# Performance work log

Measured on AMD Instinct MI355X. Metric: run time of the kernel, lower is better.

## Reference

```python
import jax, jax.numpy as jnp
import numpy as np

B, T, D, F, E, K = 2, 1024, 1024, 2048, 8, 2

def setup_inputs() -> dict:
    key = jax.random.key(0)
    ks = jax.random.split(key, 9)
    s = 0.02
    return {
        "states": jax.random.normal(ks[0], (B, T, D), dtype=jnp.float32),
        "Wg": jax.random.normal(ks[1], (D, E), dtype=jnp.float32) * s,
        "W_in": jax.random.normal(ks[2], (E, D, F), dtype=jnp.float32) * s,
        "b_in": jnp.zeros((E, F), dtype=jnp.float32),
        "W_scale": jax.random.normal(ks[3], (E, D, F), dtype=jnp.float32) * s,
        "b_scale": jnp.zeros((E, F), dtype=jnp.float32),
        "W_out": jax.random.normal(ks[4], (E, F, D), dtype=jnp.float32) * s,
        "b_out": jnp.zeros((E, D), dtype=jnp.float32),
        "num_selected": K,
    }

def reference(states, Wg, W_in, b_in, W_scale, b_scale, W_out, b_out, num_selected):
    b, t, d = states.shape
    x = states.reshape(-1, d)                      # [N, D]
    n = x.shape[0]
    # router: softmax over experts, then top-k + renormalize
    probs = jax.nn.softmax(x @ Wg, axis=-1)        # [N, E]
    topw, topi = jax.lax.top_k(probs, num_selected)  # [N, K]
    topw = topw / topw.sum(axis=-1, keepdims=True)
    # dense combine weights [N, E]: zero except selected experts
    w_full = jnp.zeros_like(probs).at[jnp.arange(n)[:, None], topi].set(topw)
    # gated-GELU expert MLPs, batched over experts
    h = jnp.einsum('nd,edf->enf', x, W_in) + b_in[:, None, :]       # [E, N, F]
    s = jnp.einsum('nd,edf->enf', x, W_scale) + b_scale[:, None, :]
    inner = jax.nn.gelu(h, approximate=False) * s                    # exact GELU (torch default)
    y = jnp.einsum('enf,efd->end', inner, W_out) + b_out[:, None, :]  # [E, N, D]
    out = jnp.einsum('end,ne->nd', y, w_full)                         # weighted combine
    return out.reshape(b, t, d)
```

## Files before the change

kernel.cpp:

```cpp
#include <hip/hip_runtime.h>
#include <hip/hip_bf16.h>
#include <math.h>

#define N_TOK 2048
#define DIM   1024
#define FF    2048
#define NEXP  8
#define NSLOT (N_TOK * 2)

typedef __attribute__((ext_vector_type(8))) short short8;
typedef __attribute__((ext_vector_type(4))) float f32x4;
typedef _Float16 half_t;
typedef __attribute__((ext_vector_type(4))) _Float16 h16x4;

__device__ __forceinline__ unsigned short f2bf(float f) {
    unsigned int u = __float_as_uint(f);
    u += 0x7FFFu + ((u >> 16) & 1u);
    return (unsigned short)(u >> 16);
}

#define GLOAD_LDS16(g, l) \
    __builtin_amdgcn_global_load_lds((const __attribute__((address_space(1))) unsigned int*)(g), \
                                     (__attribute__((address_space(3))) unsigned int*)(l), 16, 0, 0)

__global__ __launch_bounds__(256) void k_router(const float* __restrict__ x,
        const float* __restrict__ Wg, int* __restrict__ hdr,
        int* __restrict__ tok_e, float* __restrict__ tok_w) {
    int wave = threadIdx.x >> 6, lane = threadIdx.x & 63;
    int t = blockIdx.x * 4 + wave;
    float acc[NEXP];
#pragma unroll
    for (int e = 0; e < NEXP; ++e) acc[e] = 0.f;
    const float* xr = x + (size_t)t * DIM;
    for (int d = lane; d < DIM; d += 64) {
        float xv = xr[d];
        const float* wr = Wg + d * NEXP;
#pragma unroll
        for (int e = 0; e < NEXP; ++e) acc[e] += xv * wr[e];
    }
#pragma unroll
    for (int off = 32; off > 0; off >>= 1) {
#pragma unroll
        for (int e = 0; e < NEXP; ++e) acc[e] += __shfl_down(acc[e], off);
    }
    if (lane == 0) {
        int e0 = 0;
#pragma unroll
        for (int e = 1; e < NEXP; ++e) if (acc[e] > acc[e0]) e0 = e;
        int e1 = -1;
#pragma unroll
        for (int e = 0; e < NEXP; ++e) {
            if (e == e0) continue;
            if (e1 < 0 || acc[e] > acc[e1]) e1 = e;
        }
        float w0 = 1.f / (1.f + expf(acc[e1] - acc[e0]));
        tok_e[2 * t] = e0; tok_e[2 * t + 1] = e1;
        tok_w[2 * t] = w0; tok_w[2 * t + 1] = 1.f - w0;
        atomicAdd(&hdr[e0], 1);
        atomicAdd(&hdr[e1], 1);
    }
}

__global__ void k_scan(int* hdr) {
    if (threadIdx.x == 0 && blockIdx.x == 0) {
        int s = 0;
        for (int e = 0; e < NEXP; ++e) {
            hdr[16 + e] = s;
            hdr[8 + e]  = s;
            s += hdr[e];
        }
        hdr[24] = s;
    }
}

__global__ __launch_bounds__(256) void k_assign(const float* __restrict__ x,
        int* __restrict__ hdr, const int* __restrict__ tok_e,
        int* __restrict__ tok_slot, unsigned short* __restrict__ xg) {
    __shared__ int sh[2];
    int t = blockIdx.x;
    if (threadIdx.x == 0) {
        int e0 = tok_e[2 * t], e1 = tok_e[2 * t + 1];
        int p0 = atomicAdd(&hdr[8 + e0], 1);
        int p1 = atomicAdd(&hdr[8 + e1], 1);
        tok_slot[2 * t] = p0; tok_slot[2 * t + 1] = p1;
        sh[0] = p0; sh[1] = p1;
    }
    __syncthreads();
    int s0 = sh[0], s1 = sh[1];
    const float4* xr = (const float4*)(x + (size_t)t * DIM);
    float4 v = xr[threadIdx.x];
    ushort4 b;
    b.x = f2bf(v.x); b.y = f2bf(v.y); b.z = f2bf(v.z); b.w = f2bf(v.w);
    ((ushort4*)(xg + (size_t)s0 * DIM))[threadIdx.x] = b;
    ((ushort4*)(xg + (size_t)s1 * DIM))[threadIdx.x] = b;
}

__global__ __launch_bounds__(256, 4) void k_expert_hs(
        const unsigned short* __restrict__ xg,
        const float* __restrict__ Win, const float* __restrict__ Wsc,
        const float* __restrict__ b_in, const float* __restrict__ b_sc,
        const int* __restrict__ hdr, unsigned short* __restrict__ inner) {
    int e = blockIdx.z;
    int cnt = hdr[e];
    int mtile = blockIdx.y;
    if (mtile * 128 >= cnt) return;
    int base = hdr[16 + e];
    int f0 = blockIdx.x * 64;

    __shared__ unsigned short As[128 * 32];
    __shared__ unsigned short Bh[4 * 64 * 8];
    __shared__ unsigned short Bs[4 * 64 * 8];

    int tid = threadIdx.x;
    int wave = tid >> 6, lane = tid & 63;
    int lr = lane & 15, lq = lane >> 4;
    int wm = (wave >> 1) * 64, wf = (wave & 1) * 32;

    f32x4 acch[4][2], accs[4][2];
#pragma unroll
    for (int mi = 0; mi < 4; ++mi)
#pragma unroll
        for (int fi = 0; fi < 2; ++fi) {
            acch[mi][fi] = (f32x4){0.f, 0.f, 0.f, 0.f};
            accs[mi][fi] = (f32x4){0.f, 0.f, 0.f, 0.f};
        }

    const unsigned short* Arow = xg + (size_t)(base + mtile * 128) * DIM;
    int arow = wave * 16 + (lane >> 2);
    int akk  = (lane & 3) * 8;

    int bf = tid & 63, bkq = tid >> 6;
    const float* ph_base = Win + (size_t)e * DIM * FF + f0 + bf;
    const float* ps_base = Wsc + (size_t)e * DIM * FF + f0 + bf;

    unsigned hv[4], sv[4];
    {
        const float* ph = ph_base + (size_t)(bkq * 8) * FF;
        const float* ps = ps_base + (size_t)(bkq * 8) * FF;
#pragma unroll
        for (int j = 0; j < 4; ++j) {
            hv[j] = (unsigned)f2bf(ph[(size_t)(2 * j) * FF]) |
                    ((unsigned)f2bf(ph[(size_t)(2 * j + 1) * FF]) << 16);
            sv[j] = (unsigned)f2bf(ps[(size_t)(2 * j) * FF]) |
                    ((unsigned)f2bf(ps[(size_t)(2 * j + 1) * FF]) << 16);
        }
    }

    for (int k0 = 0; k0 < DIM; k0 += 32) {
        __syncthreads();
        const unsigned short* gA = Arow + (size_t)arow * DIM + k0 + akk;
        GLOAD_LDS16(gA, &As[(wave * 16) * 32]);
        GLOAD_LDS16(gA + (size_t)64 * DIM, &As[(64 + wave * 16) * 32]);
        *(uint4*)&Bh[(bkq * 64 + bf) * 8] = make_uint4(hv[0], hv[1], hv[2], hv[3]);
        *(uint4*)&Bs[(bkq * 64 + bf) * 8] = make_uint4(sv[0], sv[1], sv[2], sv[3]);
        __syncthreads();

        unsigned hvN[4], svN[4];
        bool more = (k0 + 32 < DIM);
        if (more) {
            const float* ph = ph_base + (size_t)(k0 + 32 + bkq * 8) * FF;
            const float* ps = ps_base + (size_t)(k0 + 32 + bkq * 8) * FF;
#pragma unroll
            for (int j = 0; j < 4; ++j) {
                hvN[j] = (unsigned)f2bf(ph[(size_t)(2 * j) * FF]) |
                         ((unsigned)f2bf(ph[(size_t)(2 * j + 1) * FF]) << 16);
                svN[j] = (unsigned)f2bf(ps[(size_t)(2 * j) * FF]) |
                         ((unsigned)f2bf(ps[(size_t)(2 * j + 1) * FF]) << 16);
            }
        }

        short8 af[4], bhf[2], bsf[2];
#pragma unroll
        for (int mi = 0; mi < 4; ++mi)
            af[mi] = *(const short8*)&As[(wm + mi * 16 + lr) * 32 + lq * 8];
#pragma unroll
        for (int fi = 0; fi < 2; ++fi) {
            bhf[fi] = *(const short8*)&Bh[(lq * 64 + wf + fi * 16 + lr) * 8];
            bsf[fi] = *(const short8*)&Bs[(lq * 64 + wf + fi * 16 + lr) * 8];
        }
#pragma unroll
        for (int mi = 0; mi < 4; ++mi)
#pragma unroll
            for (int fi = 0; fi < 2; ++fi) {
                acch[mi][fi] = __builtin_amdgcn_mfma_f32_16x16x32_bf16(
                    af[mi], bhf[fi], acch[mi][fi], 0, 0, 0);
                accs[mi][fi] = __builtin_amdgcn_mfma_f32_16x16x32_bf16(
                    af[mi], bsf[fi], accs[mi][fi], 0, 0, 0);
            }
        if (more) {
#pragma unroll
            for (int j = 0; j < 4; ++j) { hv[j] = hvN[j]; sv[j] = svN[j]; }
        }
    }

#pragma unroll
    for (int fi = 0; fi < 2; ++fi) {
        int f = f0 + wf + fi * 16 + lr;
        float bi = b_in[e * FF + f];
        float bs2 = b_sc[e * FF + f];
#pragma unroll
        for (int mi = 0; mi < 4; ++mi) {
#pragma unroll
            for (int r = 0; r < 4; ++r) {
                int rl = wm + mi * 16 + lq * 4 + r;
                int grow = mtile * 128 + rl;
                if (grow < cnt) {
                    float h = acch[mi][fi][r] + bi;
                    float s = accs[mi][fi][r] + bs2;
                    float g = 0.5f * h * (1.f + erff(h * 0.70710678f));
                    inner[(size_t)(base + grow) * FF + f] = f2bf(g * s);
                }
            }
        }
    }
}

__global__ __launch_bounds__(256, 4) void k_expert_out(
        const unsigned short* __restrict__ inner,
        const float* __restrict__ Wout,
        const int* __restrict__ hdr, half_t* __restrict__ pbuf) {
    int e = blockIdx.z & 7;
    int ks = blockIdx.z >> 3;
    int cnt = hdr[e];
    int mtile = blockIdx.y;
    if (mtile * 128 >= cnt) return;
    int base = hdr[16 + e];
    int d0 = blockIdx.x * 128;

    __shared__ unsigned short As[128 * 32];
    __shared__ unsigned short Bt[4 * 128 * 8];

    int tid = threadIdx.x;
    int wave = tid >> 6, lane = tid & 63;
    int lr = lane & 15, lq = lane >> 4;
    int wm = (wave >> 1) * 64, wn = (wave & 1) * 64;

    f32x4 acc[4][4];
#pragma unroll
    for (int mi = 0; mi < 4; ++mi)
#pragma unroll
        for (int ni = 0; ni < 4; ++ni) acc[mi][ni] = (f32x4){0.f, 0.f, 0.f, 0.f};

    const unsigned short* Arow = inner + (size_t)(base + mtile * 128) * FF;
    int arow = wave * 16 + (lane >> 2);
    int akk  = (lane & 3) * 8;

    int bd = tid & 127, bq = tid >> 7;
    const float* Wb = Wout + (size_t)e * FF * DIM + d0 + bd;

    int kbeg = ks * (FF / 2), kend = kbeg + FF / 2;

    unsigned wv[8];
    {
        const float* pw = Wb + (size_t)(kbeg + bq * 16) * DIM;
#pragma unroll
        for (int j = 0; j < 8; ++j)
            wv[j] = (unsigned)f2bf(pw[(size_t)(2 * j) * DIM]) |
                    ((unsigned)f2bf(pw[(size_t)(2 * j + 1) * DIM]) << 16);
    }

    for (int k0 = kbeg; k0 < kend; k0 += 32) {
        __syncthreads();
        const unsigned short* gA = Arow + (size_t)arow * FF + k0 + akk;
        GLOAD_LDS16(gA, &As[(wave * 16) * 32]);
        GLOAD_LDS16(gA + (size_t)64 * FF, &As[(64 + wave * 16) * 32]);
        *(uint4*)&Bt[((2 * bq) * 128 + bd) * 8]     = make_uint4(wv[0], wv[1], wv[2], wv[3]);
        *(uint4*)&Bt[((2 * bq + 1) * 128 + bd) * 8] = make_uint4(wv[4], wv[5], wv[6], wv[7]);
        __syncthreads();

        unsigned wvN[8];
        bool more = (k0 + 32 < kend);
        if (more) {
            const float* pw = Wb + (size_t)(k0 + 32 + bq * 16) * DIM;
#pragma unroll
            for (int j = 0; j < 8; ++j)
                wvN[j] = (unsigned)f2bf(pw[(size_t)(2 * j) * DIM]) |
                         ((unsigned)f2bf(pw[(size_t)(2 * j + 1) * DIM]) << 16);
        }

        short8 af[4], bfm[4];
#pragma unroll
        for (int mi = 0; mi < 4; ++mi)
            af[mi] = *(const short8*)&As[(wm + mi * 16 + lr) * 32 + lq * 8];
#pragma unroll
        for (int ni = 0; ni < 4; ++ni)
            bfm[ni] = *(const short8*)&Bt[(lq * 128 + wn + ni * 16 + lr) * 8];
#pragma unroll
        for (int mi = 0; mi < 4; ++mi)
#pragma unroll
            for (int ni = 0; ni < 4; ++ni)
                acc[mi][ni] = __builtin_amdgcn_mfma_f32_16x16x32_bf16(
                    af[mi], bfm[ni], acc[mi][ni], 0, 0, 0);
        if (more) {
#pragma unroll
            for (int j = 0; j < 8; ++j) wv[j] = wvN[j];
        }
    }

    half_t* P = pbuf + (size_t)ks * NSLOT * DIM;
#pragma unroll
    for (int ni = 0; ni < 4; ++ni) {
        int d = d0 + wn + ni * 16 + lr;
#pragma unroll
        for (int mi = 0; mi < 4; ++mi) {
#pragma unroll
            for (int r = 0; r < 4; ++r) {
                int rl = wm + mi * 16 + lq * 4 + r;
                int grow = mtile * 128 + rl;
                if (grow < cnt)
                    P[(size_t)(base + grow) * DIM + d] = (half_t)acc[mi][ni][r];
            }
        }
    }
}

__global__ __launch_bounds__(256) void k_combine(const half_t* __restrict__ pbuf,
        const int* __restrict__ tok_slot, const int* __restrict__ tok_e,
        const float* __restrict__ tok_w, const float* __restrict__ b_out,
        float* __restrict__ out) {
    int t = blockIdx.x;
    int d = threadIdx.x * 4;
    int s0 = tok_slot[2 * t], s1 = tok_slot[2 * t + 1];
    int e0 = tok_e[2 * t], e1 = tok_e[2 * t + 1];
    float w0 = tok_w[2 * t], w1 = tok_w[2 * t + 1];
    const half_t* pA = pbuf;
    const half_t* pB = pbuf + (size_t)NSLOT * DIM;
    h16x4 a0 = *(const h16x4*)&pA[(size_t)s0 * DIM + d];
    h16x4 a1 = *(const h16x4*)&pB[(size_t)s0 * DIM + d];
    h16x4 c0 = *(const h16x4*)&pA[(size_t)s1 * DIM + d];
    h16x4 c1 = *(const h16x4*)&pB[(size_t)s1 * DIM + d];
    float4 b0 = *(const float4*)&b_out[e0 * DIM + d];
    float4 b1 = *(const float4*)&b_out[e1 * DIM + d];
    float4 r;
    r.x = w0 * ((float)a0.x + (float)a1.x + b0.x) + w1 * ((float)c0.x + (float)c1.x + b1.x);
    r.y = w0 * ((float)a0.y + (float)a1.y + b0.y) + w1 * ((float)c0.y + (float)c1.y + b1.y);
    r.z = w0 * ((float)a0.z + (float)a1.z + b0.z) + w1 * ((float)c0.z + (float)c1.z + b1.z);
    r.w = w0 * ((float)a0.w + (float)a1.w + b0.w) + w1 * ((float)c0.w + (float)c1.w + b1.w);
    *(float4*)&out[(size_t)t * DIM + d] = r;
}

extern "C" void kernel_launch(void* const* d_in, const int* in_sizes, int n_in,
                              void* d_out, int out_size, void* d_ws, size_t ws_size,
                              hipStream_t stream) {
    (void)in_sizes; (void)n_in; (void)out_size; (void)ws_size;
    const float* x    = (const float*)d_in[0];
    const float* Wg   = (const float*)d_in[1];
    const float* Win  = (const float*)d_in[2];
    const float* b_in = (const float*)d_in[3];
    const float* Wsc  = (const float*)d_in[4];
    const float* b_sc = (const float*)d_in[5];
    const float* Wout = (const float*)d_in[6];
    const float* b_out= (const float*)d_in[7];
    float* out = (float*)d_out;

    char* ws = (char*)d_ws;
    int*   hdr      = (int*)ws;
    int*   tok_e    = (int*)(ws + 256);
    float* tok_w    = (float*)(ws + 16640);
    int*   tok_slot = (int*)(ws + 33024);
    unsigned short* xg    = (unsigned short*)(ws + 65792);
    unsigned short* inner = (unsigned short*)(ws + 65792 + 8388608);
    half_t* pbuf = (half_t*)(ws + 65792 + 8388608 + 16777216);

    hipMemsetAsync(hdr, 0, 256, stream);
    k_router<<<dim3(N_TOK / 4), dim3(256), 0, stream>>>(x, Wg, hdr, tok_e, tok_w);
    k_scan<<<dim3(1), dim3(64), 0, stream>>>(hdr);
    k_assign<<<dim3(N_TOK), dim3(256), 0, stream>>>(x, hdr, tok_e, tok_slot, xg);
    k_expert_hs<<<dim3(FF / 64, 16, NEXP), dim3(256), 0, stream>>>(xg, Win, Wsc, b_in, b_sc, hdr, inner);
    k_expert_out<<<dim3(DIM / 128, 16, NEXP * 2), dim3(256), 0, stream>>>(inner, Wout, hdr, pbuf);
    k_combine<<<dim3(N_TOK), dim3(256), 0, stream>>>(pbuf, tok_slot, tok_e, tok_w, b_out, out);
}
```

Before: 472.0 us.

## Pre-transpose expert weights to bf16 and stream all GEMM operands via direct LDS loads

Adds a transpose kernel that converts W_in, W_scale and W_out from fp32 to K-major bf16 copies in workspace. Both expert GEMMs then load A and B tiles with global_load_lds into a fragment-ordered shared layout, replacing strided per-element fp32 loads with register conversion. This is meant to cut scattered, uncoalesced weight reads and conversion work inside the GEMM loops. The cost is an extra pass that reads all weights and writes bf16 copies on every call, plus a larger workspace.

```diff
diff --git a/kernel.cpp b/kernel.cpp
--- a/kernel.cpp
+++ b/kernel.cpp
@@ -95,9 +95,41 @@
     ((ushort4*)(xg + (size_t)s1 * DIM))[threadIdx.x] = b;
 }
 
+__global__ __launch_bounds__(256) void k_transpose(
+        const float* __restrict__ Win, const float* __restrict__ Wsc,
+        const float* __restrict__ Wout, unsigned short* __restrict__ WinT,
+        unsigned short* __restrict__ WscT, unsigned short* __restrict__ WoutT) {
+    int z = blockIdx.z, tsel = z >> 3, e = z & 7;
+    int R = (tsel == 2) ? FF : DIM;
+    int C = (tsel == 2) ? DIM : FF;
+    int tr0 = blockIdx.y * 64, tc0 = blockIdx.x * 64;
+    if (tr0 >= R || tc0 >= C) return;
+    const float* src = ((tsel == 0) ? Win : (tsel == 1) ? Wsc : Wout) + (size_t)e * DIM * FF;
+    unsigned short* dst = ((tsel == 0) ? WinT : (tsel == 1) ? WscT : WoutT) + (size_t)e * DIM * FF;
+    __shared__ unsigned short T[64][68];
+    int t = threadIdx.x, tr = t >> 4, tc = (t & 15) * 4;
+#pragma unroll
+    for (int i = 0; i < 4; ++i) {
+        int r = tr + i * 16;
+        float4 v = *(const float4*)&src[(size_t)(tr0 + r) * C + tc0 + tc];
+        ushort4 b;
+        b.x = f2bf(v.x); b.y = f2bf(v.y); b.z = f2bf(v.z); b.w = f2bf(v.w);
+        *(ushort4*)&T[r][tc] = b;
+    }
+    __syncthreads();
+    int r4 = (t & 15) * 4;
+#pragma unroll
+    for (int i = 0; i < 4; ++i) {
+        int c = tr + i * 16;
+        ushort4 b;
+        b.x = T[r4][c]; b.y = T[r4 + 1][c]; b.z = T[r4 + 2][c]; b.w = T[r4 + 3][c];
+        *(ushort4*)&dst[(size_t)(tc0 + c) * R + tr0 + r4] = b;
+    }
+}
+
 __global__ __launch_bounds__(256, 4) void k_expert_hs(
         const unsigned short* __restrict__ xg,
-        const float* __restrict__ Win, const float* __restrict__ Wsc,
+        const unsigned short* __restrict__ WinT, const unsigned short* __restrict__ WscT,
         const float* __restrict__ b_in, const float* __restrict__ b_sc,
         const int* __restrict__ hdr, unsigned short* __restrict__ inner) {
     int e = blockIdx.z;
@@ -107,9 +139,9 @@
     int base = hdr[16 + e];
     int f0 = blockIdx.x * 64;
 
-    __shared__ unsigned short As[128 * 32];
-    __shared__ unsigned short Bh[4 * 64 * 8];
-    __shared__ unsigned short Bs[4 * 64 * 8];
+    __shared__ unsigned short As[8 * 512];
+    __shared__ unsigned short Bh[4 * 512];
+    __shared__ unsigned short Bs[4 * 512];
 
     int tid = threadIdx.x;
     int wave = tid >> 6, lane = tid & 63;
@@ -126,57 +158,36 @@
         }
 
     const unsigned short* Arow = xg + (size_t)(base + mtile * 128) * DIM;
-    int arow = wave * 16 + (lane >> 2);
-    int akk  = (lane & 3) * 8;
-
-    int bf = tid & 63, bkq = tid >> 6;
-    const float* ph_base = Win + (size_t)e * DIM * FF + f0 + bf;
-    const float* ps_base = Wsc + (size_t)e * DIM * FF + f0 + bf;
-
-    unsigned hv[4], sv[4];
-    {
-        const float* ph = ph_base + (size_t)(bkq * 8) * FF;
-        const float* ps = ps_base + (size_t)(bkq * 8) * FF;
-#pragma unroll
-        for (int j = 0; j < 4; ++j) {
-            hv[j] = (unsigned)f2bf(ph[(size_t)(2 * j) * FF]) |
-                    ((unsigned)f2bf(ph[(size_t)(2 * j + 1) * FF]) << 16);
-            sv[j] = (unsigned)f2bf(ps[(size_t)(2 * j) * FF]) |
-                    ((unsigned)f2bf(ps[(size_t)(2 * j + 1) * FF]) << 16);
-        }
-    }
+    const unsigned short* gA0 = Arow + (size_t)(wave * 16 + lr) * DIM + lq * 8;
+    const unsigned short* gA1 = gA0 + (size_t)64 * DIM;
+    const unsigned short* gBh = WinT + (size_t)e * DIM * FF + (size_t)(f0 + wave * 16 + lr) * DIM + lq * 8;
+    const unsigned short* gBs = WscT + (size_t)e * DIM * FF + (size_t)(f0 + wave * 16 + lr) * DIM + lq * 8;
+    unsigned short* lA0 = As + wave * 512;
+    unsigned short* lA1 = As + (4 + wave) * 512;
+    unsigned short* lBh = Bh + wave * 512;
+    unsigned short* lBs = Bs + wave * 512;
+
+    const unsigned short* rA  = As + (wm >> 4) * 512 + lq * 128 + lr * 8;
+    const unsigned short* rBh = Bh + (wf >> 4) * 512 + lq * 128 + lr * 8;
+    const unsigned short* rBs = Bs + (wf >> 4) * 512 + lq * 128 + lr * 8;
 
     for (int k0 = 0; k0 < DIM; k0 += 32) {
         __syncthreads();
-        const unsigned short* gA = Arow + (size_t)arow * DIM + k0 + akk;
-        GLOAD_LDS16(gA, &As[(wave * 16) * 32]);
-        GLOAD_LDS16(gA + (size_t)64 * DIM, &As[(64 + wave * 16) * 32]);
-        *(uint4*)&Bh[(bkq * 64 + bf) * 8] = make_uint4(hv[0], hv[1], hv[2], hv[3]);
-        *(uint4*)&Bs[(bkq * 64 + bf) * 8] = make_uint4(sv[0], sv[1], sv[2], sv[3]);
+        GLOAD_LDS16(gA0, lA0);
+        GLOAD_LDS16(gA1, lA1);
+        GLOAD_LDS16(gBh, lBh);
+        GLOAD_LDS16(gBs, lBs);
         __syncthreads();
-
-        unsigned hvN[4], svN[4];
-        bool more = (k0 + 32 < DIM);
-        if (more) {
-            const float* ph = ph_base + (size_t)(k0 + 32 + bkq * 8) * FF;
-            const float* ps = ps_base + (size_t)(k0 + 32 + bkq * 8) * FF;
-#pragma unroll
-            for (int j = 0; j < 4; ++j) {
-                hvN[j] = (unsigned)f2bf(ph[(size_t)(2 * j) * FF]) |
-                         ((unsigned)f2bf(ph[(size_t)(2 * j + 1) * FF]) << 16);
-                svN[j] = (unsigned)f2bf(ps[(size_t)(2 * j) * FF]) |
-                         ((unsigned)f2bf(ps[(size_t)(2 * j + 1) * FF]) << 16);
-            }
-        }
+        gA0 += 32; gA1 += 32; gBh += 32; gBs += 32;
 
         short8 af[4], bhf[2], bsf[2];
 #pragma unroll
         for (int mi = 0; mi < 4; ++mi)
-            af[mi] = *(const short8*)&As[(wm + mi * 16 + lr) * 32 + lq * 8];
+            af[mi] = *(const short8*)(rA + mi * 512);
 #pragma unroll
         for (int fi = 0; fi < 2; ++fi) {
-            bhf[fi] = *(const short8*)&Bh[(lq * 64 + wf + fi * 16 + lr) * 8];
-            bsf[fi] = *(const short8*)&Bs[(lq * 64 + wf + fi * 16 + lr) * 8];
+            bhf[fi] = *(const short8*)(rBh + fi * 512);
+            bsf[fi] = *(const short8*)(rBs + fi * 512);
         }
 #pragma unroll
         for (int mi = 0; mi < 4; ++mi)
@@ -187,10 +198,6 @@
                 accs[mi][fi] = __builtin_amdgcn_mfma_f32_16x16x32_bf16(
                     af[mi], bsf[fi], accs[mi][fi], 0, 0, 0);
             }
-        if (more) {
-#pragma unroll
-            for (int j = 0; j < 4; ++j) { hv[j] = hvN[j]; sv[j] = svN[j]; }
-        }
     }
 
 #pragma unroll
@@ -217,7 +224,7 @@
 
 __global__ __launch_bounds__(256, 4) void k_expert_out(
         const unsigned short* __restrict__ inner,
-        const float* __restrict__ Wout,
+        const unsigned short* __restrict__ WoutT,
         const int* __restrict__ hdr, half_t* __restrict__ pbuf) {
     int e = blockIdx.z & 7;
     int ks = blockIdx.z >> 3;
@@ -227,8 +234,8 @@
     int base = hdr[16 + e];
     int d0 = blockIdx.x * 128;
 
-    __shared__ unsigned short As[128 * 32];
-    __shared__ unsigned short Bt[4 * 128 * 8];
+    __shared__ unsigned short As[8 * 512];
+    __shared__ unsigned short Bt[8 * 512];
 
     int tid = threadIdx.x;
     int wave = tid >> 6, lane = tid & 63;
@@ -241,60 +248,42 @@
 #pragma unroll
         for (int ni = 0; ni < 4; ++ni) acc[mi][ni] = (f32x4){0.f, 0.f, 0.f, 0.f};
 
+    int kbeg = ks * (FF / 2);
     const unsigned short* Arow = inner + (size_t)(base + mtile * 128) * FF;
-    int arow = wave * 16 + (lane >> 2);
-    int akk  = (lane & 3) * 8;
-
-    int bd = tid & 127, bq = tid >> 7;
-    const float* Wb = Wout + (size_t)e * FF * DIM + d0 + bd;
-
-    int kbeg = ks * (FF / 2), kend = kbeg + FF / 2;
-
-    unsigned wv[8];
-    {
-        const float* pw = Wb + (size_t)(kbeg + bq * 16) * DIM;
-#pragma unroll
-        for (int j = 0; j < 8; ++j)
-            wv[j] = (unsigned)f2bf(pw[(size_t)(2 * j) * DIM]) |
-                    ((unsigned)f2bf(pw[(size_t)(2 * j + 1) * DIM]) << 16);
-    }
-
-    for (int k0 = kbeg; k0 < kend; k0 += 32) {
+    const unsigned short* gA0 = Arow + (size_t)(wave * 16 + lr) * FF + kbeg + lq * 8;
+    const unsigned short* gA1 = gA0 + (size_t)64 * FF;
+    const unsigned short* gB0 = WoutT + (size_t)e * DIM * FF + (size_t)(d0 + wave * 16 + lr) * FF + kbeg + lq * 8;
+    const unsigned short* gB1 = gB0 + (size_t)64 * FF;
+    unsigned short* lA0 = As + wave * 512;
+    unsigned short* lA1 = As + (4 + wave) * 512;
+    unsigned short* lB0 = Bt + wave * 512;
+    unsigned short* lB1 = Bt + (4 + wave) * 512;
+
+    const unsigned short* rA = As + (wm >> 4) * 512 + lq * 128 + lr * 8;
+    const unsigned short* rB = Bt + (wn >> 4) * 512 + lq * 128 + lr * 8;
+
+    for (int ki = 0; ki < FF / 2; ki += 32) {
         __syncthreads();
-        const unsigned short* gA = Arow + (size_t)arow * FF + k0 + akk;
-        GLOAD_LDS16(gA, &As[(wave * 16) * 32]);
-        GLOAD_LDS16(gA + (size_t)64 * FF, &As[(64 + wave * 16) * 32]);
-        *(uint4*)&Bt[((2 * bq) * 128 + bd) * 8]     = make_uint4(wv[0], wv[1], wv[2], wv[3]);
-        *(uint4*)&Bt[((2 * bq + 1) * 128 + bd) * 8] = make_uint4(wv[4], wv[5], wv[6], wv[7]);
+        GLOAD_LDS16(gA0, lA0);
+        GLOAD_LDS16(gA1, lA1);
+        GLOAD_LDS16(gB0, lB0);
+        GLOAD_LDS16(gB1, lB1);
         __syncthreads();
-
-        unsigned wvN[8];
-        bool more = (k0 + 32 < kend);
-        if (more) {
-            const float* pw = Wb + (size_t)(k0 + 32 + bq * 16) * DIM;
-#pragma unroll
-            for (int j = 0; j < 8; ++j)
-                wvN[j] = (unsigned)f2bf(pw[(size_t)(2 * j) * DIM]) |
-                         ((unsigned)f2bf(pw[(size_t)(2 * j + 1) * DIM]) << 16);
-        }
+        gA0 += 32; gA1 += 32; gB0 += 32; gB1 += 32;
 
         short8 af[4], bfm[4];
 #pragma unroll
         for (int mi = 0; mi < 4; ++mi)
-            af[mi] = *(const short8*)&As[(wm + mi * 16 + lr) * 32 + lq * 8];
+            af[mi] = *(const short8*)(rA + mi * 512);
 #pragma unroll
         for (int ni = 0; ni < 4; ++ni)
-            bfm[ni] = *(const short8*)&Bt[(lq * 128 + wn + ni * 16 + lr) * 8];
+            bfm[ni] = *(const short8*)(rB + ni * 512);
 #pragma unroll
         for (int mi = 0; mi < 4; ++mi)
 #pragma unroll
             for (int ni = 0; ni < 4; ++ni)
                 acc[mi][ni] = __builtin_amdgcn_mfma_f32_16x16x32_bf16(
                     af[mi], bfm[ni], acc[mi][ni], 0, 0, 0);
-        if (more) {
-#pragma unroll
-            for (int j = 0; j < 8; ++j) wv[j] = wvN[j];
-        }
     }
 
     half_t* P = pbuf + (size_t)ks * NSLOT * DIM;
@@ -359,14 +348,18 @@
     float* tok_w    = (float*)(ws + 16640);
     int*   tok_slot = (int*)(ws + 33024);
     unsigned short* xg    = (unsigned short*)(ws + 65792);
-    unsigned short* inner = (unsigned short*)(ws + 65792 + 8388608);
-    half_t* pbuf = (half_t*)(ws + 65792 + 8388608 + 16777216);
+    unsigned short* inner = (unsigned short*)(ws + 8454400);
+    half_t*         pbuf  = (half_t*)        (ws + 25231616);
+    unsigned short* WinT  = (unsigned short*)(ws + 42008832);
+    unsigned short* WscT  = (unsigned short*)(ws + 75563264);
+    unsigned short* WoutT = (unsigned short*)(ws + 109117696);
 
     hipMemsetAsync(hdr, 0, 256, stream);
+    k_transpose<<<dim3(32, 32, 24), dim3(256), 0, stream>>>(Win, Wsc, Wout, WinT, WscT, WoutT);
     k_router<<<dim3(N_TOK / 4), dim3(256), 0, stream>>>(x, Wg, hdr, tok_e, tok_w);
     k_scan<<<dim3(1), dim3(64), 0, stream>>>(hdr);
     k_assign<<<dim3(N_TOK), dim3(256), 0, stream>>>(x, hdr, tok_e, tok_slot, xg);
-    k_expert_hs<<<dim3(FF / 64, 16, NEXP), dim3(256), 0, stream>>>(xg, Win, Wsc, b_in, b_sc, hdr, inner);
-    k_expert_out<<<dim3(DIM / 128, 16, NEXP * 2), dim3(256), 0, stream>>>(inner, Wout, hdr, pbuf);
+    k_expert_hs<<<dim3(FF / 64, 16, NEXP), dim3(256), 0, stream>>>(xg, WinT, WscT, b_in, b_sc, hdr, inner);
+    k_expert_out<<<dim3(DIM / 128, 16, NEXP * 2), dim3(256), 0, stream>>>(inner, WoutT, hdr, pbuf);
     k_combine<<<dim3(N_TOK), dim3(256), 0, stream>>>(pbuf, tok_slot, tok_e, tok_w, b_out, out);
 }
```

Result: slower. 502.6 us (+6.5%).
